# Optimization experiments

Hardware: AMD Instinct MI355X
Metric: run time of the kernel (lower is better)

The kernel has to match this reference:

```python
import jax, jax.numpy as jnp
import numpy as np

B, SPLIT, D = 4096, 32, 256
UNITS = 256  # must equal D for the final view in the original module


def setup_inputs() -> dict:
    key = jax.random.key(0)
    kx, kw, kb = jax.random.split(key, 3)
    x = jax.random.normal(kx, (B, SPLIT, D), dtype=jnp.float32)
    W = jax.random.normal(kw, (SPLIT, D, UNITS), dtype=jnp.float32) * 0.02
    b = jax.random.normal(kb, (SPLIT, UNITS), dtype=jnp.float32) * 0.02
    return {"x": x, "W": W, "b": b}


def reference(x, W, b):
    # Original: loop over split dim, per-split matmul + bias + activation, concat,
    # then view(B, split, input_dim). Fused here as a single batched einsum.
    out = jnp.einsum('bsd,sdu->bsu', x, W) + b[None, :, :]
    out = jax.nn.relu(out)  # activation
    # concat along dim 1 then view(B, split, input_dim) == [B, SPLIT, UNITS] since UNITS == D
    return out
```

## Files before the change

kernel.cpp:

```cpp
#include <hip/hip_runtime.h>
#include <hip/hip_bf16.h>

typedef __attribute__((ext_vector_type(8))) short bf16x8;
typedef __attribute__((ext_vector_type(4))) float f32x4;

#define SPLITN 32
#define DDIM   256
#define UNITS  256
#define BROWS  4096

#define BM 128
#define BN 128
#define BK 64

static __device__ __forceinline__ ushort f2bf(float f) {
    __hip_bfloat16 h = __float2bfloat16(f);
    return *reinterpret_cast<ushort*>(&h);
}

__global__ __launch_bounds__(256) void wt_prep(const float* __restrict__ W,
                                               ushort* __restrict__ Wt) {
    __shared__ float tile[64][65];
    const int s  = blockIdx.z;
    const int d0 = blockIdx.y * 64;
    const int u0 = blockIdx.x * 64;
    const int t  = threadIdx.x;

    const float* Ws = W + s * 65536;
    #pragma unroll
    for (int i = 0; i < 4; ++i) {
        int f  = t + i * 256;
        int d  = f >> 4;
        int uq = f & 15;
        f32x4 v = *reinterpret_cast<const f32x4*>(Ws + (d0 + d) * 256 + u0 + uq * 4);
        tile[d][uq * 4 + 0] = v[0];
        tile[d][uq * 4 + 1] = v[1];
        tile[d][uq * 4 + 2] = v[2];
        tile[d][uq * 4 + 3] = v[3];
    }
    __syncthreads();

    ushort* Wts = Wt + s * 65536;
    #pragma unroll
    for (int i = 0; i < 4; ++i) {
        int g  = t + i * 256;
        int u  = g >> 4;
        int dq = g & 15;
        uint lo = (uint)f2bf(tile[dq * 4 + 0][u]) | ((uint)f2bf(tile[dq * 4 + 1][u]) << 16);
        uint hi = (uint)f2bf(tile[dq * 4 + 2][u]) | ((uint)f2bf(tile[dq * 4 + 3][u]) << 16);
        uint2 val; val.x = lo; val.y = hi;
        *reinterpret_cast<uint2*>(Wts + (u0 + u) * 256 + d0 + dq * 4) = val;
    }
}

__global__ __launch_bounds__(256) void lc_gemm(const float* __restrict__ x,
                                               const ushort* __restrict__ Wt,
                                               const float* __restrict__ bias,
                                               float* __restrict__ out) {
    const int bid = blockIdx.x;
    const int swz = (bid & 7) * 256 + (bid >> 3);
    const int s   = swz >> 6;
    const int r   = swz & 63;
    const int mt  = r >> 1;
    const int nt  = r & 1;
    const int m0  = mt * BM;
    const int u0  = nt * BN;

    __shared__ ushort As[BM * BK];
    __shared__ ushort Bs[BN * BK];

    const int t  = threadIdx.x;
    const int w  = t >> 6, l = t & 63;
    const int wr = w >> 1, wc = w & 1;
    const int lr = l & 15, lg = l >> 4;

    f32x4 acc[4][4];
    #pragma unroll
    for (int i = 0; i < 4; ++i)
        #pragma unroll
        for (int j = 0; j < 4; ++j) {
            f32x4 z = {0.f, 0.f, 0.f, 0.f};
            acc[i][j] = z;
        }

    const float*  xA = x  + (long)m0 * 8192 + s * 256;
    const ushort* WB = Wt + s * 65536 + u0 * 256;

    for (int kt = 0; kt < 4; ++kt) {
        const int k0 = kt * BK;

        #pragma unroll
        for (int i = 0; i < 8; ++i) {
            int f  = t + i * 256;
            int m  = f >> 4;
            int kq = f & 15;
            f32x4 v = *reinterpret_cast<const f32x4*>(xA + m * 8192 + k0 + kq * 4);
            uint lo = (uint)f2bf(v[0]) | ((uint)f2bf(v[1]) << 16);
            uint hi = (uint)f2bf(v[2]) | ((uint)f2bf(v[3]) << 16);
            int e = (m * BK + kq * 4) ^ ((m & 7) << 3);
            uint2 val; val.x = lo; val.y = hi;
            *reinterpret_cast<uint2*>(&As[e]) = val;
        }
        #pragma unroll
        for (int i = 0; i < 4; ++i) {
            int f  = t + i * 256;
            int u  = f >> 3;
            int dq = f & 7;
            int4 v = *reinterpret_cast<const int4*>(WB + u * 256 + k0 + dq * 8);
            int e = (u * BK + dq * 8) ^ ((u & 7) << 3);
            *reinterpret_cast<int4*>(&Bs[e]) = v;
        }
        __syncthreads();

        #pragma unroll
        for (int kk = 0; kk < BK; kk += 32) {
            bf16x8 af[4], bf[4];
            #pragma unroll
            for (int mi = 0; mi < 4; ++mi) {
                int row = wr * 64 + mi * 16 + lr;
                int e = (row * BK + kk + lg * 8) ^ ((row & 7) << 3);
                af[mi] = *reinterpret_cast<const bf16x8*>(&As[e]);
            }
            #pragma unroll
            for (int ni = 0; ni < 4; ++ni) {
                int row = wc * 64 + ni * 16 + lr;
                int e = (row * BK + kk + lg * 8) ^ ((row & 7) << 3);
                bf[ni] = *reinterpret_cast<const bf16x8*>(&Bs[e]);
            }
            #pragma unroll
            for (int mi = 0; mi < 4; ++mi)
                #pragma unroll
                for (int ni = 0; ni < 4; ++ni)
                    acc[mi][ni] = __builtin_amdgcn_mfma_f32_16x16x32_bf16(
                        af[mi], bf[ni], acc[mi][ni], 0, 0, 0);
        }
        __syncthreads();
    }

    #pragma unroll
    for (int ni = 0; ni < 4; ++ni) {
        int col = u0 + wc * 64 + ni * 16 + lr;
        float bv = bias[s * 256 + col];
        #pragma unroll
        for (int mi = 0; mi < 4; ++mi) {
            int row0 = m0 + wr * 64 + mi * 16 + lg * 4;
            #pragma unroll
            for (int rr = 0; rr < 4; ++rr) {
                float v = acc[mi][ni][rr] + bv;
                out[(long)(row0 + rr) * 8192 + s * 256 + col] = fmaxf(v, 0.f);
            }
        }
    }
}

__global__ void naive_lc(const float* __restrict__ x, const float* __restrict__ W,
                         const float* __restrict__ b, float* __restrict__ out,
                         int total) {
    int i = blockIdx.x * blockDim.x + threadIdx.x;
    if (i >= total) return;
    int u = i & 255;
    int s = (i >> 8) & 31;
    int bi = i >> 13;
    const float* xr = x + (long)bi * 8192 + s * 256;
    const float* wc = W + s * 65536 + u;
    float acc = 0.f;
    #pragma unroll 4
    for (int d = 0; d < 256; ++d) acc += xr[d] * wc[d * 256];
    out[i] = fmaxf(acc + b[s * 256 + u], 0.f);
}

extern "C" void kernel_launch(void* const* d_in, const int* in_sizes, int n_in,
                              void* d_out, int out_size, void* d_ws, size_t ws_size,
                              hipStream_t stream) {
    const float* x = (const float*)d_in[0];
    const float* W = (const float*)d_in[1];
    const float* b = (const float*)d_in[2];
    float* out = (float*)d_out;

    const size_t wt_bytes = (size_t)SPLITN * DDIM * UNITS * sizeof(ushort);
    if (ws_size >= wt_bytes) {
        ushort* Wt = (ushort*)d_ws;
        wt_prep<<<dim3(4, 4, 32), 256, 0, stream>>>(W, Wt);
        lc_gemm<<<dim3(2048), 256, 0, stream>>>(x, Wt, b, out);
    } else {
        int total = BROWS * SPLITN * UNITS;
        naive_lc<<<(total + 255) / 256, 256, 0, stream>>>(x, W, b, out, total);
    }
}
```

Before: 276.7 us.

## Double-buffer LDS with register prefetch and reshape tiles to 64x256

Switches the GEMM to a 64x256 output tile with BK=32 so each block covers the full unit dimension, which means x is read and converted once per row block instead of twice. It adds double-buffered shared memory with register prefetch of the next K slice, overlapping global loads with MFMA work and needing only one barrier per iteration. It also changes the LDS swizzle pattern and requests three blocks per CU through launch bounds. The cost is more K iterations with a smaller BK and a risk of register pressure under the occupancy hint.

```diff
diff --git a/kernel.cpp b/kernel.cpp
--- a/kernel.cpp
+++ b/kernel.cpp
@@ -9,13 +9,18 @@
 #define UNITS  256
 #define BROWS  4096
 
-#define BM 128
-#define BN 128
-#define BK 64
+#define BM 64
+#define BN 256
+#define BK 32
+#define NKT (DDIM / BK)
 
 static __device__ __forceinline__ ushort f2bf(float f) {
     __hip_bfloat16 h = __float2bfloat16(f);
     return *reinterpret_cast<ushort*>(&h);
+}
+
+static __device__ __forceinline__ int swz(int row, int e) {
+    return (row * BK + e) ^ (((row >> 1) & 3) << 3);
 }
 
 __global__ __launch_bounds__(256) void wt_prep(const float* __restrict__ W,
@@ -53,26 +58,29 @@
     }
 }
 
-__global__ __launch_bounds__(256) void lc_gemm(const float* __restrict__ x,
-                                               const ushort* __restrict__ Wt,
-                                               const float* __restrict__ bias,
-                                               float* __restrict__ out) {
+__global__ __launch_bounds__(256, 3) void lc_gemm(const float* __restrict__ x,
+                                                  const ushort* __restrict__ Wt,
+                                                  const float* __restrict__ bias,
+                                                  float* __restrict__ out) {
     const int bid = blockIdx.x;
-    const int swz = (bid & 7) * 256 + (bid >> 3);
-    const int s   = swz >> 6;
-    const int r   = swz & 63;
-    const int mt  = r >> 1;
-    const int nt  = r & 1;
+    const int sw  = (bid & 7) * 256 + (bid >> 3);
+    const int s   = sw >> 6;
+    const int mt  = sw & 63;
     const int m0  = mt * BM;
-    const int u0  = nt * BN;
-
-    __shared__ ushort As[BM * BK];
-    __shared__ ushort Bs[BN * BK];
+
+    __shared__ ushort As[2][BM * BK];
+    __shared__ ushort Bs[2][BN * BK];
 
     const int t  = threadIdx.x;
-    const int w  = t >> 6, l = t & 63;
-    const int wr = w >> 1, wc = w & 1;
+    const int wc = t >> 6;
+    const int l  = t & 63;
     const int lr = l & 15, lg = l >> 4;
+
+    const int am0 = t >> 3,  akq = t & 7;
+    const int bu0 = t >> 2,  bdq = t & 3;
+
+    const float*  xA = x  + (long)m0 * 8192 + s * 256;
+    const ushort* WB = Wt + s * 65536;
 
     f32x4 acc[4][4];
     #pragma unroll
@@ -83,67 +91,83 @@
             acc[i][j] = z;
         }
 
-    const float*  xA = x  + (long)m0 * 8192 + s * 256;
-    const ushort* WB = Wt + s * 65536 + u0 * 256;
-
-    for (int kt = 0; kt < 4; ++kt) {
-        const int k0 = kt * BK;
-
-        #pragma unroll
-        for (int i = 0; i < 8; ++i) {
-            int f  = t + i * 256;
-            int m  = f >> 4;
-            int kq = f & 15;
-            f32x4 v = *reinterpret_cast<const f32x4*>(xA + m * 8192 + k0 + kq * 4);
-            uint lo = (uint)f2bf(v[0]) | ((uint)f2bf(v[1]) << 16);
-            uint hi = (uint)f2bf(v[2]) | ((uint)f2bf(v[3]) << 16);
-            int e = (m * BK + kq * 4) ^ ((m & 7) << 3);
-            uint2 val; val.x = lo; val.y = hi;
-            *reinterpret_cast<uint2*>(&As[e]) = val;
-        }
-        #pragma unroll
-        for (int i = 0; i < 4; ++i) {
-            int f  = t + i * 256;
-            int u  = f >> 3;
-            int dq = f & 7;
-            int4 v = *reinterpret_cast<const int4*>(WB + u * 256 + k0 + dq * 8);
-            int e = (u * BK + dq * 8) ^ ((u & 7) << 3);
-            *reinterpret_cast<int4*>(&Bs[e]) = v;
-        }
-        __syncthreads();
-
-        #pragma unroll
-        for (int kk = 0; kk < BK; kk += 32) {
-            bf16x8 af[4], bf[4];
+    {
+        f32x4 av0 = *reinterpret_cast<const f32x4*>(xA + am0 * 8192 + akq * 4);
+        f32x4 av1 = *reinterpret_cast<const f32x4*>(xA + (am0 + 32) * 8192 + akq * 4);
+        int4  bv0 = *reinterpret_cast<const int4*>(WB + bu0 * 256 + bdq * 8);
+        int4  bv1 = *reinterpret_cast<const int4*>(WB + (bu0 + 64) * 256 + bdq * 8);
+        int4  bv2 = *reinterpret_cast<const int4*>(WB + (bu0 + 128) * 256 + bdq * 8);
+        int4  bv3 = *reinterpret_cast<const int4*>(WB + (bu0 + 192) * 256 + bdq * 8);
+        uint2 w0, w1;
+        w0.x = (uint)f2bf(av0[0]) | ((uint)f2bf(av0[1]) << 16);
+        w0.y = (uint)f2bf(av0[2]) | ((uint)f2bf(av0[3]) << 16);
+        w1.x = (uint)f2bf(av1[0]) | ((uint)f2bf(av1[1]) << 16);
+        w1.y = (uint)f2bf(av1[2]) | ((uint)f2bf(av1[3]) << 16);
+        *reinterpret_cast<uint2*>(&As[0][swz(am0,      akq * 4)]) = w0;
+        *reinterpret_cast<uint2*>(&As[0][swz(am0 + 32, akq * 4)]) = w1;
+        *reinterpret_cast<int4*>(&Bs[0][swz(bu0,       bdq * 8)]) = bv0;
+        *reinterpret_cast<int4*>(&Bs[0][swz(bu0 + 64,  bdq * 8)]) = bv1;
+        *reinterpret_cast<int4*>(&Bs[0][swz(bu0 + 128, bdq * 8)]) = bv2;
+        *reinterpret_cast<int4*>(&Bs[0][swz(bu0 + 192, bdq * 8)]) = bv3;
+    }
+    __syncthreads();
+
+    #pragma unroll
+    for (int kt = 0; kt < NKT; ++kt) {
+        const int cur = kt & 1, nxt = cur ^ 1;
+
+        f32x4 av0, av1; int4 bv0, bv1, bv2, bv3;
+        if (kt < NKT - 1) {
+            const int k0 = (kt + 1) * BK;
+            av0 = *reinterpret_cast<const f32x4*>(xA + am0 * 8192 + k0 + akq * 4);
+            av1 = *reinterpret_cast<const f32x4*>(xA + (am0 + 32) * 8192 + k0 + akq * 4);
+            bv0 = *reinterpret_cast<const int4*>(WB + bu0 * 256 + k0 + bdq * 8);
+            bv1 = *reinterpret_cast<const int4*>(WB + (bu0 + 64) * 256 + k0 + bdq * 8);
+            bv2 = *reinterpret_cast<const int4*>(WB + (bu0 + 128) * 256 + k0 + bdq * 8);
+            bv3 = *reinterpret_cast<const int4*>(WB + (bu0 + 192) * 256 + k0 + bdq * 8);
+        }
+
+        bf16x8 af[4], bf[4];
+        #pragma unroll
+        for (int mi = 0; mi < 4; ++mi) {
+            int row = mi * 16 + lr;
+            af[mi] = *reinterpret_cast<const bf16x8*>(&As[cur][swz(row, lg * 8)]);
+        }
+        #pragma unroll
+        for (int ni = 0; ni < 4; ++ni) {
+            int row = wc * 64 + ni * 16 + lr;
+            bf[ni] = *reinterpret_cast<const bf16x8*>(&Bs[cur][swz(row, lg * 8)]);
+        }
+        #pragma unroll
+        for (int mi = 0; mi < 4; ++mi)
             #pragma unroll
-            for (int mi = 0; mi < 4; ++mi) {
-                int row = wr * 64 + mi * 16 + lr;
-                int e = (row * BK + kk + lg * 8) ^ ((row & 7) << 3);
-                af[mi] = *reinterpret_cast<const bf16x8*>(&As[e]);
-            }
-            #pragma unroll
-            for (int ni = 0; ni < 4; ++ni) {
-                int row = wc * 64 + ni * 16 + lr;
-                int e = (row * BK + kk + lg * 8) ^ ((row & 7) << 3);
-                bf[ni] = *reinterpret_cast<const bf16x8*>(&Bs[e]);
-            }
-            #pragma unroll
-            for (int mi = 0; mi < 4; ++mi)
-                #pragma unroll
-                for (int ni = 0; ni < 4; ++ni)
-                    acc[mi][ni] = __builtin_amdgcn_mfma_f32_16x16x32_bf16(
-                        af[mi], bf[ni], acc[mi][ni], 0, 0, 0);
-        }
-        __syncthreads();
+            for (int ni = 0; ni < 4; ++ni)
+                acc[mi][ni] = __builtin_amdgcn_mfma_f32_16x16x32_bf16(
+                    af[mi], bf[ni], acc[mi][ni], 0, 0, 0);
+
+        if (kt < NKT - 1) {
+            uint2 w0, w1;
+            w0.x = (uint)f2bf(av0[0]) | ((uint)f2bf(av0[1]) << 16);
+            w0.y = (uint)f2bf(av0[2]) | ((uint)f2bf(av0[3]) << 16);
+            w1.x = (uint)f2bf(av1[0]) | ((uint)f2bf(av1[1]) << 16);
+            w1.y = (uint)f2bf(av1[2]) | ((uint)f2bf(av1[3]) << 16);
+            *reinterpret_cast<uint2*>(&As[nxt][swz(am0,      akq * 4)]) = w0;
+            *reinterpret_cast<uint2*>(&As[nxt][swz(am0 + 32, akq * 4)]) = w1;
+            *reinterpret_cast<int4*>(&Bs[nxt][swz(bu0,       bdq * 8)]) = bv0;
+            *reinterpret_cast<int4*>(&Bs[nxt][swz(bu0 + 64,  bdq * 8)]) = bv1;
+            *reinterpret_cast<int4*>(&Bs[nxt][swz(bu0 + 128, bdq * 8)]) = bv2;
+            *reinterpret_cast<int4*>(&Bs[nxt][swz(bu0 + 192, bdq * 8)]) = bv3;
+            __syncthreads();
+        }
     }
 
     #pragma unroll
     for (int ni = 0; ni < 4; ++ni) {
-        int col = u0 + wc * 64 + ni * 16 + lr;
+        int col = wc * 64 + ni * 16 + lr;
         float bv = bias[s * 256 + col];
         #pragma unroll
         for (int mi = 0; mi < 4; ++mi) {
-            int row0 = m0 + wr * 64 + mi * 16 + lg * 4;
+            int row0 = m0 + mi * 16 + lg * 4;
             #pragma unroll
             for (int rr = 0; rr < 4; ++rr) {
                 float v = acc[mi][ni][rr] + bv;
```

After: 290.9 us. +5.1%, slower.

## Keep weights in registers and stream x directly into MFMA without LDS

Applied to the files above, without the earlier changes.

Replaces the LDS-tiled GEMM with a kernel where each wave holds its full-K weight slice in registers and streams x rows from global memory directly into MFMA fragments. It prefetches the next row tile and uses nontemporal stores for the output. The aim is to remove the LDS staging, the barriers and the duplicate x loads across N tiles. In exchange it needs very high register use, has fewer blocks, and relies on cache to share x reads across the four waves.

```diff
diff --git a/kernel.cpp b/kernel.cpp
--- a/kernel.cpp
+++ b/kernel.cpp
@@ -9,13 +9,21 @@
 #define UNITS  256
 #define BROWS  4096
 
-#define BM 128
-#define BN 128
-#define BK 64
+#define NIT  16
+#define MCHN (BROWS / (NIT * 16))
 
 static __device__ __forceinline__ ushort f2bf(float f) {
     __hip_bfloat16 h = __float2bfloat16(f);
     return *reinterpret_cast<ushort*>(&h);
+}
+
+static __device__ __forceinline__ bf16x8 cvt8(f32x4 lo, f32x4 hi) {
+    union { uint u32[4]; bf16x8 v; } r;
+    r.u32[0] = (uint)f2bf(lo[0]) | ((uint)f2bf(lo[1]) << 16);
+    r.u32[1] = (uint)f2bf(lo[2]) | ((uint)f2bf(lo[3]) << 16);
+    r.u32[2] = (uint)f2bf(hi[0]) | ((uint)f2bf(hi[1]) << 16);
+    r.u32[3] = (uint)f2bf(hi[2]) | ((uint)f2bf(hi[3]) << 16);
+    return r.v;
 }
 
 __global__ __launch_bounds__(256) void wt_prep(const float* __restrict__ W,
@@ -53,101 +61,79 @@
     }
 }
 
-__global__ __launch_bounds__(256) void lc_gemm(const float* __restrict__ x,
-                                               const ushort* __restrict__ Wt,
-                                               const float* __restrict__ bias,
-                                               float* __restrict__ out) {
+__global__ __launch_bounds__(256, 2) void lc_gemm(const float* __restrict__ x,
+                                                  const ushort* __restrict__ Wt,
+                                                  const float* __restrict__ bias,
+                                                  float* __restrict__ out) {
     const int bid = blockIdx.x;
-    const int swz = (bid & 7) * 256 + (bid >> 3);
-    const int s   = swz >> 6;
-    const int r   = swz & 63;
-    const int mt  = r >> 1;
-    const int nt  = r & 1;
-    const int m0  = mt * BM;
-    const int u0  = nt * BN;
-
-    __shared__ ushort As[BM * BK];
-    __shared__ ushort Bs[BN * BK];
+    const int sw  = (bid & 7) * 64 + (bid >> 3);
+    const int s   = sw >> 4;
+    const int mc  = sw & 15;
+    const int m0  = mc * (NIT * 16);
 
     const int t  = threadIdx.x;
-    const int w  = t >> 6, l = t & 63;
-    const int wr = w >> 1, wc = w & 1;
-    const int lr = l & 15, lg = l >> 4;
+    const int wc = t >> 6;
+    const int l  = t & 63;
+    const int lr = l & 15;
+    const int lg = l >> 4;
 
-    f32x4 acc[4][4];
+    bf16x8 Bf[4][8];
+    {
+        const ushort* wb = Wt + s * 65536 + (wc * 64 + lr) * 256 + lg * 8;
+        #pragma unroll
+        for (int ni = 0; ni < 4; ++ni)
+            #pragma unroll
+            for (int k = 0; k < 8; ++k)
+                Bf[ni][k] = *reinterpret_cast<const bf16x8*>(wb + ni * (16 * 256) + k * 32);
+    }
+
+    float bv[4];
     #pragma unroll
-    for (int i = 0; i < 4; ++i)
+    for (int ni = 0; ni < 4; ++ni)
+        bv[ni] = bias[s * 256 + wc * 64 + ni * 16 + lr];
+
+    const float* xp = x + (long)(m0 + lr) * 8192 + s * 256 + lg * 8;
+
+    f32x4 a[8][2];
+    #pragma unroll
+    for (int k = 0; k < 8; ++k) {
+        a[k][0] = *reinterpret_cast<const f32x4*>(xp + k * 32);
+        a[k][1] = *reinterpret_cast<const f32x4*>(xp + k * 32 + 4);
+    }
+
+    float* op = out + (long)(m0 + lg * 4) * 8192 + s * 256 + wc * 64 + lr;
+
+    for (int it = 0; it < NIT; ++it) {
+        const int nit = (it + 1 < NIT) ? (it + 1) : it;
+        const float* xn = xp + (long)nit * (16 * 8192);
+
+        f32x4 acc[4];
         #pragma unroll
-        for (int j = 0; j < 4; ++j) {
+        for (int ni = 0; ni < 4; ++ni) {
             f32x4 z = {0.f, 0.f, 0.f, 0.f};
-            acc[i][j] = z;
+            acc[ni] = z;
         }
 
-    const float*  xA = x  + (long)m0 * 8192 + s * 256;
-    const ushort* WB = Wt + s * 65536 + u0 * 256;
-
-    for (int kt = 0; kt < 4; ++kt) {
-        const int k0 = kt * BK;
+        #pragma unroll
+        for (int k = 0; k < 8; ++k) {
+            bf16x8 af = cvt8(a[k][0], a[k][1]);
+            f32x4 n0 = *reinterpret_cast<const f32x4*>(xn + k * 32);
+            f32x4 n1 = *reinterpret_cast<const f32x4*>(xn + k * 32 + 4);
+            #pragma unroll
+            for (int ni = 0; ni < 4; ++ni)
+                acc[ni] = __builtin_amdgcn_mfma_f32_16x16x32_bf16(
+                    af, Bf[ni][k], acc[ni], 0, 0, 0);
+            a[k][0] = n0;
+            a[k][1] = n1;
+        }
 
         #pragma unroll
-        for (int i = 0; i < 8; ++i) {
-            int f  = t + i * 256;
-            int m  = f >> 4;
-            int kq = f & 15;
-            f32x4 v = *reinterpret_cast<const f32x4*>(xA + m * 8192 + k0 + kq * 4);
-            uint lo = (uint)f2bf(v[0]) | ((uint)f2bf(v[1]) << 16);
-            uint hi = (uint)f2bf(v[2]) | ((uint)f2bf(v[3]) << 16);
-            int e = (m * BK + kq * 4) ^ ((m & 7) << 3);
-            uint2 val; val.x = lo; val.y = hi;
-            *reinterpret_cast<uint2*>(&As[e]) = val;
-        }
-        #pragma unroll
-        for (int i = 0; i < 4; ++i) {
-            int f  = t + i * 256;
-            int u  = f >> 3;
-            int dq = f & 7;
-            int4 v = *reinterpret_cast<const int4*>(WB + u * 256 + k0 + dq * 8);
-            int e = (u * BK + dq * 8) ^ ((u & 7) << 3);
-            *reinterpret_cast<int4*>(&Bs[e]) = v;
-        }
-        __syncthreads();
-
-        #pragma unroll
-        for (int kk = 0; kk < BK; kk += 32) {
-            bf16x8 af[4], bf[4];
-            #pragma unroll
-            for (int mi = 0; mi < 4; ++mi) {
-                int row = wr * 64 + mi * 16 + lr;
-                int e = (row * BK + kk + lg * 8) ^ ((row & 7) << 3);
-                af[mi] = *reinterpret_cast<const bf16x8*>(&As[e]);
-            }
-            #pragma unroll
-            for (int ni = 0; ni < 4; ++ni) {
-                int row = wc * 64 + ni * 16 + lr;
-                int e = (row * BK + kk + lg * 8) ^ ((row & 7) << 3);
-                bf[ni] = *reinterpret_cast<const bf16x8*>(&Bs[e]);
-            }
-            #pragma unroll
-            for (int mi = 0; mi < 4; ++mi)
-                #pragma unroll
-                for (int ni = 0; ni < 4; ++ni)
-                    acc[mi][ni] = __builtin_amdgcn_mfma_f32_16x16x32_bf16(
-                        af[mi], bf[ni], acc[mi][ni], 0, 0, 0);
-        }
-        __syncthreads();
-    }
-
-    #pragma unroll
-    for (int ni = 0; ni < 4; ++ni) {
-        int col = u0 + wc * 64 + ni * 16 + lr;
-        float bv = bias[s * 256 + col];
-        #pragma unroll
-        for (int mi = 0; mi < 4; ++mi) {
-            int row0 = m0 + wr * 64 + mi * 16 + lg * 4;
+        for (int ni = 0; ni < 4; ++ni) {
             #pragma unroll
             for (int rr = 0; rr < 4; ++rr) {
-                float v = acc[mi][ni][rr] + bv;
-                out[(long)(row0 + rr) * 8192 + s * 256 + col] = fmaxf(v, 0.f);
+                float v = fmaxf(acc[ni][rr] + bv[ni], 0.f);
+                __builtin_nontemporal_store(
+                    v, op + (long)(it * 16 + rr) * 8192 + ni * 16);
             }
         }
     }
@@ -181,7 +167,7 @@
     if (ws_size >= wt_bytes) {
         ushort* Wt = (ushort*)d_ws;
         wt_prep<<<dim3(4, 4, 32), 256, 0, stream>>>(W, Wt);
-        lc_gemm<<<dim3(2048), 256, 0, stream>>>(x, Wt, b, out);
+        lc_gemm<<<dim3(SPLITN * MCHN), 256, 0, stream>>>(x, Wt, b, out);
     } else {
         int total = BROWS * SPLITN * UNITS;
         naive_lc<<<(total + 255) / 256, 256, 0, stream>>>(x, W, b, out, total);
```

Result: faster. 270.1 us (-2.4%).
